# Performance work log

Measured on AMD Instinct MI355X. Metric: run time of the kernel, lower is better.

The kernel has to match this reference:

```python
import jax, jax.numpy as jnp
import numpy as np

C = 32           # max_channels (in == out == 32, stride 1)
K = 3            # base kernel size
EXP_NITER = 5    # ConvExponential iterations -> effective kernel 11x11
POWER_IT = 3     # FantasticFour power iterations
B, H, W = 16, 256, 256


def _l2n(x):
    # L2Normalize over all dims (applied on store via right_inverse and again on read; idempotent)
    return x / (jnp.sqrt(jnp.sum(x * x)) + 1e-12)


def _skew(k):
    # K - flip(K^T, spatial)
    return k - jnp.flip(jnp.transpose(k, (1, 0, 2, 3)), axis=(2, 3))


def _fantastic_four(kernel, u1, u2, u3, u4):
    u1, u2, u3, u4 = map(_l2n, (u1, u2, u3, u4))
    for _ in range(POWER_IT):
        v1 = _l2n(jnp.sum(kernel * u1, axis=(1, 3), keepdims=True))
        u1 = _l2n(jnp.sum(kernel * v1, axis=(0, 2), keepdims=True))
        v2 = _l2n(jnp.sum(kernel * u2, axis=(1, 2), keepdims=True))
        u2 = _l2n(jnp.sum(kernel * v2, axis=(0, 3), keepdims=True))
        v3 = _l2n(jnp.sum(kernel * u3, axis=(1, 2, 3), keepdims=True))
        u3 = _l2n(jnp.sum(kernel * v3, axis=0, keepdims=True))
        v4 = _l2n(jnp.sum(kernel * u4, axis=(0, 2, 3), keepdims=True))
        u4 = _l2n(jnp.sum(kernel * v4, axis=1, keepdims=True))
    sg = jax.lax.stop_gradient  # sigmas use detached u/v, grad only via kernel
    s1 = jnp.sum(kernel * sg(u1) * sg(v1))
    s2 = jnp.sum(kernel * sg(u2) * sg(v2))
    s3 = jnp.sum(kernel * sg(u3) * sg(v3))
    s4 = jnp.sum(kernel * sg(u4) * sg(v4))
    sigma = jnp.minimum(jnp.minimum(s1, s2), jnp.minimum(s3, s4))
    return kernel / sigma


def _conv_exp(kernel):
    # kernel_global = I + K + K*K/2! + ... (kernel composition = full spatial convolution)
    p = (K - 1) // 2
    ident = jnp.pad(jnp.eye(C, dtype=kernel.dtype)[:, :, None, None],
                    ((0, 0), (0, 0), (p, p), (p, p)))
    kg = kernel + ident            # (C, C, K, K)
    ki = kernel
    rhs = jnp.flip(kernel, axis=(2, 3))  # flip -> lax correlation becomes full convolution
    for i in range(2, EXP_NITER + 1):
        # out[o,d,y,x] = sum_{c,p,q} ki[c,d,y-p,x-q] * kernel[o,c,p,q]
        inp = jnp.transpose(ki, (1, 0, 2, 3))  # (d, c, h, w) as NCHW
        out = jax.lax.conv_general_dilated(
            inp, rhs, window_strides=(1, 1),
            padding=[(K - 1, K - 1), (K - 1, K - 1)],
            dimension_numbers=('NCHW', 'OIHW', 'NCHW'))
        ki = jnp.transpose(out, (1, 0, 2, 3)) / float(i)
        kg = jnp.pad(kg, ((0, 0), (0, 0), (p, p), (p, p))) + ki
    return kg  # (C, C, 11, 11) for K=3, EXP_NITER=5


def reference(x, weight_raw, bias, u1, u2, u3, u4):
    w = _conv_exp(_fantastic_four(_skew(weight_raw), u1, u2, u3, u4))
    pad = w.shape[2] // 2  # 5
    z = jnp.pad(x, ((0, 0), (0, 0), (pad, pad), (pad, pad)), mode='wrap')  # circular
    z = jax.lax.conv_general_dilated(
        z, w, window_strides=(1, 1), padding='VALID',
        dimension_numbers=('NCHW', 'OIHW', 'NCHW'))
    return z + bias[None, :, None, None]


def setup_inputs() -> dict:
    key = jax.random.key(0)
    ks = jax.random.split(key, 7)
    return {
        'x': jax.random.normal(ks[0], (B, C, H, W), dtype=jnp.float32),
        'weight_raw': jax.random.normal(ks[1], (C, C, K, K), dtype=jnp.float32),
        'bias': jax.random.normal(ks[2], (C,), dtype=jnp.float32),
        'u1': jax.random.normal(ks[3], (1, C, 1, K), dtype=jnp.float32),
        'u2': jax.random.normal(ks[4], (1, C, K, 1), dtype=jnp.float32),
        'u3': jax.random.normal(ks[5], (1, C, K, K), dtype=jnp.float32),
        'u4': jax.random.normal(ks[6], (C, 1, K, K), dtype=jnp.float32),
    }
```

## Files before the change

### kernel.cpp

```cpp
#include <hip/hip_runtime.h>
#include <math.h>

typedef __bf16 bf16x8 __attribute__((ext_vector_type(8)));
typedef float f32x16 __attribute__((ext_vector_type(16)));
typedef unsigned int uint4v __attribute__((ext_vector_type(4)));

__device__ __forceinline__ unsigned short bf16_rne(float f) {
    unsigned u = __float_as_uint(f);
    unsigned r = u + 0x7fffu + ((u >> 16) & 1u);
    return (unsigned short)(r >> 16);
}
__device__ __forceinline__ float bf16_to_f(unsigned short h) {
    return __uint_as_float(((unsigned)h) << 16);
}

__device__ __forceinline__ float block_sum256(float v, float* red) {
    #pragma unroll
    for (int off = 32; off > 0; off >>= 1)
        v += __shfl_down(v, off, 64);
    const int tid = threadIdx.x;
    if ((tid & 63) == 0) red[tid >> 6] = v;
    __syncthreads();
    float tot = red[0] + red[1] + red[2] + red[3];
    __syncthreads();
    return tot;
}

__device__ __forceinline__ void l2n_lds(float* a, int n, float* red) {
    float s = 0.f;
    for (int i = threadIdx.x; i < n; i += 256) s += a[i] * a[i];
    const float tot = block_sum256(s, red);
    const float sc = 1.0f / (sqrtf(tot) + 1e-12f);
    for (int i = threadIdx.x; i < n; i += 256) a[i] *= sc;
    __syncthreads();
}

__global__ __launch_bounds__(256) void ff_kernel(
    const float* __restrict__ wr,
    const float* __restrict__ u1g, const float* __restrict__ u2g,
    const float* __restrict__ u3g, const float* __restrict__ u4g,
    float* __restrict__ kf_out)
{
    __shared__ float ks[9216];
    __shared__ float u1[96], v1[96], u2[96], v2[96];
    __shared__ float u3[288], u4[288], v3[32], v4[32];
    __shared__ float red[8];
    const int tid = threadIdx.x;

    for (int i = tid; i < 9216; i += 256) {
        int q  = i % 3;
        int p  = (i / 3) % 3;
        int ic = (i / 9) % 32;
        int oc = i / 288;
        ks[i] = wr[i] - wr[ic * 288 + oc * 9 + (2 - p) * 3 + (2 - q)];
    }
    if (tid < 96) { u1[tid] = u1g[tid]; u2[tid] = u2g[tid]; }
    for (int i = tid; i < 288; i += 256) { u3[i] = u3g[i]; u4[i] = u4g[i]; }
    __syncthreads();
    l2n_lds(u1, 96, red);
    l2n_lds(u2, 96, red);
    l2n_lds(u3, 288, red);
    l2n_lds(u4, 288, red);

    for (int it = 0; it < 3; ++it) {
        if (tid < 96) {
            int o = tid / 3, p = tid % 3;
            float s = 0.f;
            for (int i = 0; i < 32; ++i)
                for (int q = 0; q < 3; ++q)
                    s += ks[o * 288 + i * 9 + p * 3 + q] * u1[i * 3 + q];
            v1[tid] = s;
        }
        __syncthreads();
        l2n_lds(v1, 96, red);
        if (tid < 96) {
            int i = tid / 3, q = tid % 3;
            float s = 0.f;
            for (int o = 0; o < 32; ++o)
                for (int p = 0; p < 3; ++p)
                    s += ks[o * 288 + i * 9 + p * 3 + q] * v1[o * 3 + p];
            u1[tid] = s;
        }
        __syncthreads();
        l2n_lds(u1, 96, red);
        if (tid < 96) {
            int o = tid / 3, q = tid % 3;
            float s = 0.f;
            for (int i = 0; i < 32; ++i)
                for (int p = 0; p < 3; ++p)
                    s += ks[o * 288 + i * 9 + p * 3 + q] * u2[i * 3 + p];
            v2[tid] = s;
        }
        __syncthreads();
        l2n_lds(v2, 96, red);
        if (tid < 96) {
            int i = tid / 3, p = tid % 3;
            float s = 0.f;
            for (int o = 0; o < 32; ++o)
                for (int q = 0; q < 3; ++q)
                    s += ks[o * 288 + i * 9 + p * 3 + q] * v2[o * 3 + q];
            u2[tid] = s;
        }
        __syncthreads();
        l2n_lds(u2, 96, red);
        if (tid < 32) {
            float s = 0.f;
            for (int i = 0; i < 32; ++i)
                for (int pq = 0; pq < 9; ++pq)
                    s += ks[tid * 288 + i * 9 + pq] * u3[i * 9 + pq];
            v3[tid] = s;
        }
        __syncthreads();
        l2n_lds(v3, 32, red);
        for (int j = tid; j < 288; j += 256) {
            float s = 0.f;
            for (int o = 0; o < 32; ++o)
                s += ks[o * 288 + j] * v3[o];
            u3[j] = s;
        }
        __syncthreads();
        l2n_lds(u3, 288, red);
        if (tid < 32) {
            float s = 0.f;
            for (int o = 0; o < 32; ++o)
                for (int pq = 0; pq < 9; ++pq)
                    s += ks[o * 288 + tid * 9 + pq] * u4[o * 9 + pq];
            v4[tid] = s;
        }
        __syncthreads();
        l2n_lds(v4, 32, red);
        for (int j = tid; j < 288; j += 256) {
            int o = j / 9, pq = j - o * 9;
            float s = 0.f;
            for (int i = 0; i < 32; ++i)
                s += ks[o * 288 + i * 9 + pq] * v4[i];
            u4[j] = s;
        }
        __syncthreads();
        l2n_lds(u4, 288, red);
    }

    float p1 = 0.f, p2 = 0.f, p3 = 0.f, p4 = 0.f;
    for (int idx = tid; idx < 9216; idx += 256) {
        int q = idx % 3;
        int p = (idx / 3) % 3;
        int i = (idx / 9) % 32;
        int o = idx / 288;
        float k = ks[idx];
        p1 += k * u1[i * 3 + q] * v1[o * 3 + p];
        p2 += k * u2[i * 3 + p] * v2[o * 3 + q];
        p3 += k * u3[i * 9 + p * 3 + q] * v3[o];
        p4 += k * u4[o * 9 + p * 3 + q] * v4[i];
    }
    float s1 = block_sum256(p1, red);
    float s2 = block_sum256(p2, red);
    float s3 = block_sum256(p3, red);
    float s4 = block_sum256(p4, red);
    float sigma = fminf(fminf(s1, s2), fminf(s3, s4));
    for (int idx = tid; idx < 9216; idx += 256)
        kf_out[idx] = ks[idx] / sigma;
}

__global__ void initacc_kernel(const float* __restrict__ kf, float* __restrict__ wacc) {
    int idx = blockIdx.x * 256 + threadIdx.x;
    if (idx >= 123904) return;
    int o = idx / 3872;
    int rem = idx - o * 3872;
    int c = rem / 121;
    int yx = rem - c * 121;
    int y = yx / 11, x = yx - y * 11;
    float v = (o == c && y == 5 && x == 5) ? 1.0f : 0.0f;
    if (y >= 4 && y <= 6 && x >= 4 && x <= 6)
        v += kf[o * 288 + c * 9 + (y - 4) * 3 + (x - 4)];
    wacc[idx] = v;
}

__global__ void expstep_kernel(const float* __restrict__ kf, const float* __restrict__ ki,
                               float* __restrict__ ko, float* __restrict__ wacc,
                               int S, float scale)
{
    const int S2 = S + 2;
    const int off = (11 - S2) >> 1;
    const int o = blockIdx.x >> 5;
    const int d = blockIdx.x & 31;
    for (int yx = threadIdx.x; yx < S2 * S2; yx += blockDim.x) {
        int y = yx / S2, xx = yx - y * S2;
        float s = 0.f;
        for (int c = 0; c < 32; ++c) {
            const float* kfo = kf + o * 288 + c * 9;
            const float* kic = ki + (c * 32 + d) * S * S;
            #pragma unroll
            for (int p = 0; p < 3; ++p) {
                int yy = y - p;
                if (yy < 0 || yy >= S) continue;
                #pragma unroll
                for (int q = 0; q < 3; ++q) {
                    int xq = xx - q;
                    if (xq < 0 || xq >= S) continue;
                    s += kfo[p * 3 + q] * kic[yy * S + xq];
                }
            }
        }
        s *= scale;
        ko[(o * 32 + d) * S2 * S2 + yx] = s;
        wacc[(o * 32 + d) * 121 + (y + off) * 11 + (xx + off)] += s;
    }
}

__global__ void wprep_kernel(const float* __restrict__ wacc, uint4v* __restrict__ wbuf) {
    int idx = blockIdx.x * 256 + threadIdx.x;
    if (idx >= 30976) return;
    int lane  = idx & 63;
    int split = (idx >> 6) & 1;
    int ch    = (idx >> 7) & 1;
    int tap   = idx >> 8;
    int o     = lane & 31;
    int cbase = ch * 16 + ((lane >> 5) << 3);
    unsigned short v[8];
    #pragma unroll
    for (int j = 0; j < 8; ++j) {
        float w = wacc[o * 3872 + (cbase + j) * 121 + tap];
        unsigned short h = bf16_rne(w);
        v[j] = split ? bf16_rne(w - bf16_to_f(h)) : h;
    }
    uint4v u;
    u.x = (unsigned)v[0] | ((unsigned)v[1] << 16);
    u.y = (unsigned)v[2] | ((unsigned)v[3] << 16);
    u.z = (unsigned)v[4] | ((unsigned)v[5] << 16);
    u.w = (unsigned)v[6] | ((unsigned)v[7] << 16);
    wbuf[idx] = u;
}

__global__ __launch_bounds__(256, 2) void conv_mfma_kernel(
    const float* __restrict__ x, const uint4v* __restrict__ wbuf,
    const float* __restrict__ bias, float* __restrict__ out)
{
    __shared__ unsigned short shi[1092 * 16];
    __shared__ unsigned short slo[1092 * 16];
    __shared__ float biasS[32];

    const int b    = blockIdx.z;
    const int Y0   = blockIdx.y << 4;
    const int X0   = blockIdx.x << 5;
    const int tid  = threadIdx.x;
    const int lane = tid & 63;
    const int ywave = (tid >> 6) << 2;
    const int myoff = ((lane & 31) << 1) + (lane >> 5);

    if (tid < 32) biasS[tid] = bias[tid];

    f32x16 acc[4];
    #pragma unroll
    for (int s = 0; s < 4; ++s)
        #pragma unroll
        for (int r = 0; r < 16; ++r) acc[s][r] = 0.f;

    const uint4v* ph = (const uint4v*)shi;
    const uint4v* pl = (const uint4v*)slo;

    for (int chlf = 0; chlf < 2; ++chlf) {
        __syncthreads();
        const float* xb = x + (((size_t)(b * 32 + chlf * 16)) << 16);
        for (int pix = tid; pix < 1092; pix += 256) {
            int r = pix / 42, s = pix - r * 42;
            int gy = (Y0 + r - 5) & 255;
            int gx = (X0 + s - 5) & 255;
            const float* xp = xb + (gy << 8) + gx;
            unsigned short hv[16], lv[16];
            #pragma unroll
            for (int cc = 0; cc < 16; ++cc) {
                float v = xp[(size_t)cc << 16];
                unsigned short h = bf16_rne(v);
                hv[cc] = h;
                lv[cc] = bf16_rne(v - bf16_to_f(h));
            }
            uint4v u;
            u.x = (unsigned)hv[0] | ((unsigned)hv[1] << 16);
            u.y = (unsigned)hv[2] | ((unsigned)hv[3] << 16);
            u.z = (unsigned)hv[4] | ((unsigned)hv[5] << 16);
            u.w = (unsigned)hv[6] | ((unsigned)hv[7] << 16);
            *(uint4v*)&shi[pix * 16] = u;
            u.x = (unsigned)hv[8]  | ((unsigned)hv[9]  << 16);
            u.y = (unsigned)hv[10] | ((unsigned)hv[11] << 16);
            u.z = (unsigned)hv[12] | ((unsigned)hv[13] << 16);
            u.w = (unsigned)hv[14] | ((unsigned)hv[15] << 16);
            *(uint4v*)&shi[pix * 16 + 8] = u;
            u.x = (unsigned)lv[0] | ((unsigned)lv[1] << 16);
            u.y = (unsigned)lv[2] | ((unsigned)lv[3] << 16);
            u.z = (unsigned)lv[4] | ((unsigned)lv[5] << 16);
            u.w = (unsigned)lv[6] | ((unsigned)lv[7] << 16);
            *(uint4v*)&slo[pix * 16] = u;
            u.x = (unsigned)lv[8]  | ((unsigned)lv[9]  << 16);
            u.y = (unsigned)lv[10] | ((unsigned)lv[11] << 16);
            u.z = (unsigned)lv[12] | ((unsigned)lv[13] << 16);
            u.w = (unsigned)lv[14] | ((unsigned)lv[15] << 16);
            *(uint4v*)&slo[pix * 16 + 8] = u;
        }
        __syncthreads();

        const int wb0 = chlf * 128 + lane;
        uint4v a0 = wbuf[wb0];
        uint4v a1 = wbuf[wb0 + 64];
        #pragma unroll 1
        for (int tap = 0; tap < 121; ++tap) {
            bf16x8 Ahi = __builtin_bit_cast(bf16x8, a0);
            bf16x8 Alo = __builtin_bit_cast(bf16x8, a1);
            if (tap < 120) {
                a0 = wbuf[wb0 + (tap + 1) * 256];
                a1 = wbuf[wb0 + (tap + 1) * 256 + 64];
            }
            int p = tap / 11, q = tap - p * 11;
            int u0 = ((ywave + p) * 42 + q) * 2 + myoff;
            #pragma unroll
            for (int s = 0; s < 4; ++s) {
                bf16x8 Bh = __builtin_bit_cast(bf16x8, ph[u0 + s * 84]);
                bf16x8 Bl = __builtin_bit_cast(bf16x8, pl[u0 + s * 84]);
                acc[s] = __builtin_amdgcn_mfma_f32_32x32x16_bf16(Ahi, Bh, acc[s], 0, 0, 0);
                acc[s] = __builtin_amdgcn_mfma_f32_32x32x16_bf16(Alo, Bh, acc[s], 0, 0, 0);
                acc[s] = __builtin_amdgcn_mfma_f32_32x32x16_bf16(Ahi, Bl, acc[s], 0, 0, 0);
            }
        }
    }

    const int colx = X0 + (lane & 31);
    const int half = lane >> 5;
    #pragma unroll
    for (int s = 0; s < 4; ++s) {
        int y = Y0 + ywave + s;
        #pragma unroll
        for (int r = 0; r < 16; ++r) {
            int o = (r & 3) + ((r >> 2) << 3) + (half << 2);
            out[(((size_t)(b * 32 + o)) << 16) + (y << 8) + colx] = acc[s][r] + biasS[o];
        }
    }
}

extern "C" void kernel_launch(void* const* d_in, const int* in_sizes, int n_in,
                              void* d_out, int out_size, void* d_ws, size_t ws_size,
                              hipStream_t stream) {
    const float* x    = (const float*)d_in[0];
    const float* wraw = (const float*)d_in[1];
    const float* bias = (const float*)d_in[2];
    const float* u1   = (const float*)d_in[3];
    const float* u2   = (const float*)d_in[4];
    const float* u3   = (const float*)d_in[5];
    const float* u4   = (const float*)d_in[6];
    float* out = (float*)d_out;

    float* ws   = (float*)d_ws;
    float* kf   = ws;
    float* bufA = kf + 9216;
    float* bufB = bufA + 123904;
    float* wacc = bufB + 123904;
    uint4v* wbuf = (uint4v*)(wacc + 123904);

    ff_kernel<<<1, 256, 0, stream>>>(wraw, u1, u2, u3, u4, kf);
    initacc_kernel<<<484, 256, 0, stream>>>(kf, wacc);
    expstep_kernel<<<1024, 128, 0, stream>>>(kf, kf,   bufA, wacc, 3, 0.5f);
    expstep_kernel<<<1024, 128, 0, stream>>>(kf, bufA, bufB, wacc, 5, 1.0f / 3.0f);
    expstep_kernel<<<1024, 128, 0, stream>>>(kf, bufB, bufA, wacc, 7, 0.25f);
    expstep_kernel<<<1024, 128, 0, stream>>>(kf, bufA, bufB, wacc, 9, 0.2f);
    wprep_kernel<<<121, 256, 0, stream>>>(wacc, wbuf);

    conv_mfma_kernel<<<dim3(8, 16, 16), 256, 0, stream>>>(x, wbuf, bias, out);
}
```

Before: 924.7 us.

## Reorder taps column-major with rolling B-fragment reuse and swizzled LDS layout

Measured after the change: 939.2 us. No clear change (+1.6%).

```diff
diff --git a/kernel.cpp b/kernel.cpp
--- a/kernel.cpp
+++ b/kernel.cpp
@@ -239,13 +239,14 @@
     __shared__ unsigned short slo[1092 * 16];
     __shared__ float biasS[32];
 
-    const int b    = blockIdx.z;
-    const int Y0   = blockIdx.y << 4;
-    const int X0   = blockIdx.x << 5;
-    const int tid  = threadIdx.x;
-    const int lane = tid & 63;
+    const int b     = blockIdx.z;
+    const int Y0    = blockIdx.y << 4;
+    const int X0    = blockIdx.x << 5;
+    const int tid   = threadIdx.x;
+    const int lane  = tid & 63;
     const int ywave = (tid >> 6) << 2;
-    const int myoff = ((lane & 31) << 1) + (lane >> 5);
+    const int laneN = lane & 31;
+    const int kh    = lane >> 5;
 
     if (tid < 32) biasS[tid] = bias[tid];
 
@@ -274,62 +275,80 @@
                 hv[cc] = h;
                 lv[cc] = bf16_rne(v - bf16_to_f(h));
             }
+            const int bsw = (pix >> 2) & 1;
             uint4v u;
             u.x = (unsigned)hv[0] | ((unsigned)hv[1] << 16);
             u.y = (unsigned)hv[2] | ((unsigned)hv[3] << 16);
             u.z = (unsigned)hv[4] | ((unsigned)hv[5] << 16);
             u.w = (unsigned)hv[6] | ((unsigned)hv[7] << 16);
-            *(uint4v*)&shi[pix * 16] = u;
+            ((uint4v*)shi)[2 * pix + bsw] = u;
             u.x = (unsigned)hv[8]  | ((unsigned)hv[9]  << 16);
             u.y = (unsigned)hv[10] | ((unsigned)hv[11] << 16);
             u.z = (unsigned)hv[12] | ((unsigned)hv[13] << 16);
             u.w = (unsigned)hv[14] | ((unsigned)hv[15] << 16);
-            *(uint4v*)&shi[pix * 16 + 8] = u;
+            ((uint4v*)shi)[2 * pix + (1 ^ bsw)] = u;
             u.x = (unsigned)lv[0] | ((unsigned)lv[1] << 16);
             u.y = (unsigned)lv[2] | ((unsigned)lv[3] << 16);
             u.z = (unsigned)lv[4] | ((unsigned)lv[5] << 16);
             u.w = (unsigned)lv[6] | ((unsigned)lv[7] << 16);
-            *(uint4v*)&slo[pix * 16] = u;
+            ((uint4v*)slo)[2 * pix + bsw] = u;
             u.x = (unsigned)lv[8]  | ((unsigned)lv[9]  << 16);
             u.y = (unsigned)lv[10] | ((unsigned)lv[11] << 16);
             u.z = (unsigned)lv[12] | ((unsigned)lv[13] << 16);
             u.w = (unsigned)lv[14] | ((unsigned)lv[15] << 16);
-            *(uint4v*)&slo[pix * 16 + 8] = u;
+            ((uint4v*)slo)[2 * pix + (1 ^ bsw)] = u;
         }
         __syncthreads();
 
         const int wb0 = chlf * 128 + lane;
-        uint4v a0 = wbuf[wb0];
-        uint4v a1 = wbuf[wb0 + 64];
         #pragma unroll 1
-        for (int tap = 0; tap < 121; ++tap) {
-            bf16x8 Ahi = __builtin_bit_cast(bf16x8, a0);
-            bf16x8 Alo = __builtin_bit_cast(bf16x8, a1);
-            if (tap < 120) {
-                a0 = wbuf[wb0 + (tap + 1) * 256];
-                a1 = wbuf[wb0 + (tap + 1) * 256 + 64];
+        for (int q = 0; q < 11; ++q) {
+            uint4v Bh[4], Bl[4];
+            #pragma unroll
+            for (int r = 0; r < 4; ++r) {
+                int pix = (ywave + r) * 42 + q + laneN;
+                int u = 2 * pix + (kh ^ ((pix >> 2) & 1));
+                Bh[r] = ph[u];
+                Bl[r] = pl[u];
             }
-            int p = tap / 11, q = tap - p * 11;
-            int u0 = ((ywave + p) * 42 + q) * 2 + myoff;
+            uint4v a0 = wbuf[wb0 + q * 256];
+            uint4v a1 = wbuf[wb0 + q * 256 + 64];
             #pragma unroll
-            for (int s = 0; s < 4; ++s) {
-                bf16x8 Bh = __builtin_bit_cast(bf16x8, ph[u0 + s * 84]);
-                bf16x8 Bl = __builtin_bit_cast(bf16x8, pl[u0 + s * 84]);
-                acc[s] = __builtin_amdgcn_mfma_f32_32x32x16_bf16(Ahi, Bh, acc[s], 0, 0, 0);
-                acc[s] = __builtin_amdgcn_mfma_f32_32x32x16_bf16(Alo, Bh, acc[s], 0, 0, 0);
-                acc[s] = __builtin_amdgcn_mfma_f32_32x32x16_bf16(Ahi, Bl, acc[s], 0, 0, 0);
+            for (int p = 0; p < 11; ++p) {
+                bf16x8 Ahi = __builtin_bit_cast(bf16x8, a0);
+                bf16x8 Alo = __builtin_bit_cast(bf16x8, a1);
+                if (p < 10) {
+                    int tap = (p + 1) * 11 + q;
+                    a0 = wbuf[wb0 + tap * 256];
+                    a1 = wbuf[wb0 + tap * 256 + 64];
+                }
+                #pragma unroll
+                for (int s = 0; s < 4; ++s) {
+                    const int slot = (p + s) & 3;
+                    bf16x8 Bhs = __builtin_bit_cast(bf16x8, Bh[slot]);
+                    bf16x8 Bls = __builtin_bit_cast(bf16x8, Bl[slot]);
+                    acc[s] = __builtin_amdgcn_mfma_f32_32x32x16_bf16(Ahi, Bhs, acc[s], 0, 0, 0);
+                    acc[s] = __builtin_amdgcn_mfma_f32_32x32x16_bf16(Alo, Bhs, acc[s], 0, 0, 0);
+                    acc[s] = __builtin_amdgcn_mfma_f32_32x32x16_bf16(Ahi, Bls, acc[s], 0, 0, 0);
+                }
+                if (p < 10) {
+                    int rr = p + 4;
+                    int pix = (ywave + rr) * 42 + q + laneN;
+                    int u = 2 * pix + (kh ^ ((pix >> 2) & 1));
+                    Bh[p & 3] = ph[u];
+                    Bl[p & 3] = pl[u];
+                }
             }
         }
     }
 
-    const int colx = X0 + (lane & 31);
-    const int half = lane >> 5;
+    const int colx = X0 + laneN;
     #pragma unroll
     for (int s = 0; s < 4; ++s) {
         int y = Y0 + ywave + s;
         #pragma unroll
         for (int r = 0; r < 16; ++r) {
-            int o = (r & 3) + ((r >> 2) << 3) + (half << 2);
+            int o = (r & 3) + ((r >> 2) << 3) + (kh << 2);
             out[(((size_t)(b * 32 + o)) << 16) + (y << 8) + colx] = acc[s][r] + biasS[o];
         }
     }
```
